# Kernel tuning notes

Hardware: AMD Instinct MI355X
Metric: run time of the kernel (lower is better)

## Reference

```python
import jax, jax.numpy as jnp
import numpy as np

B, V, LP, LO = 256, 128000, 1024, 256


def setup_inputs() -> dict:
    key = jax.random.key(0)
    ks = jax.random.split(key, 11)
    logits = jax.random.normal(ks[0], (B, V), jnp.float32) * 4.0
    presence_penalties = jax.random.uniform(ks[1], (B,), jnp.float32, 0.0, 0.5)
    frequency_penalties = jax.random.uniform(ks[2], (B,), jnp.float32, 0.0, 0.5)
    repetition_penalties = jax.random.uniform(ks[3], (B,), jnp.float32, 1.0, 1.3)
    temperatures = jax.random.uniform(ks[4], (B,), jnp.float32, 0.5, 1.5)
    top_ps = jax.random.uniform(ks[5], (B,), jnp.float32, 0.8, 1.0)
    top_as = jax.random.uniform(ks[6], (B,), jnp.float32, 0.0, 0.2)
    min_ps = jax.random.uniform(ks[7], (B,), jnp.float32, 0.0, 0.1)
    prompt_tokens = jax.random.randint(ks[8], (B, LP), 0, V, jnp.int32)
    output_tokens = jax.random.randint(ks[9], (B, LO), 0, V, jnp.int32)
    top_ks = jax.random.randint(ks[10], (B,), 1, 2048, jnp.int32)
    return dict(logits=logits, presence_penalties=presence_penalties,
                frequency_penalties=frequency_penalties,
                repetition_penalties=repetition_penalties,
                temperatures=temperatures, top_ps=top_ps, top_as=top_as,
                min_ps=min_ps, prompt_tokens=prompt_tokens,
                output_tokens=output_tokens, top_ks=top_ks)


def _bin_counts(tokens, num_seqs, vocab):
    # scatter-add histogram of token ids per row (torch _get_bin_counts_and_mask)
    rows = jnp.arange(num_seqs)[:, None]
    counts = jnp.zeros((num_seqs, vocab), jnp.int32).at[rows, tokens].add(1)
    return counts, counts > 0


def reference(logits, presence_penalties, frequency_penalties,
              repetition_penalties, temperatures, top_ps, top_as, min_ps,
              prompt_tokens, output_tokens, top_ks):
    num_seqs, vocab = logits.shape

    # ---- _apply_penalties ----
    _, prompt_mask = _bin_counts(prompt_tokens, num_seqs, vocab)
    out_counts, out_mask = _bin_counts(output_tokens, num_seqs, vocab)
    rep = jnp.where(prompt_mask | out_mask, repetition_penalties[:, None], 1.0)
    logits = jnp.where(logits > 0, logits / rep, logits * rep)
    logits = logits - frequency_penalties[:, None] * out_counts.astype(logits.dtype)
    logits = logits - presence_penalties[:, None] * out_mask.astype(logits.dtype)

    # ---- _apply_temperature (static path; dynatemp mins/maxs == 0) ----
    temps = jnp.where(temperatures == 0.0, 1.0, temperatures)
    logits = logits / temps[:, None]

    # ---- _apply_alphabet_soup: top-p / top-k / top-a / min-p ----
    order = jnp.argsort(-logits, axis=-1)               # descending sort order
    logits_sort = jnp.take_along_axis(logits, order, axis=-1)
    probs_sort = jax.nn.softmax(logits_sort, axis=-1)
    probs_sum = jnp.cumsum(probs_sort, axis=-1) - probs_sort  # exclusive cumsum
    p_top = probs_sort[:, :1]
    threshold = jnp.maximum(p_top * min_ps[:, None],
                            (p_top * p_top) * top_as[:, None])
    mask = (probs_sort < threshold) | (probs_sum > top_ps[:, None])
    mask = mask.at[:, 0].set(False)                     # always keep argmax
    mask = mask | (jnp.arange(vocab)[None, :] >= top_ks[:, None])  # per-row top-k
    logits_sort = jnp.where(mask, -jnp.inf, logits_sort)

    inv = jnp.argsort(order, axis=-1)                   # inverse permutation
    return jnp.take_along_axis(logits_sort, inv, axis=-1)
```

## Files before the change

### kernel.cpp

```cpp
#include <hip/hip_runtime.h>
#include <hip/hip_fp16.h>
#include <cstdint>

#define NV 128000
#define NROWS 256
#define NLP 1024
#define NLO 256
#define HASH_SZ 4096
#define HEMPTY 0xFFFFFFFFu
#define NBINS 2048
#define GCAP 4096
#define M0 40.0f
#define LOG2E 1.44269504f
#define MASK16 0xFBFFu
#define MASK32 0xFBFFFBFFu

#define HIST_BYTES (NROWS * NBINS * 4)
#define WS_ZERO_BYTES (HIST_BYTES + NROWS * 4)

__device__ __forceinline__ int lbin(float l) {
    int b = (int)((l + 32.0f) * 32.0f);
    return max(0, min(b, NBINS - 1));
}

__device__ __forceinline__ float dec_bf16(uint32_t b) {
    union { uint32_t u; float f; } c; c.u = b << 16; return c.f;
}
__device__ __forceinline__ float dec_fp16(uint32_t h) {
    uint32_t s = h >> 15, e = (h >> 10) & 31u, m = h & 1023u;
    union { uint32_t u; float f; } c;
    if (e == 0) { c.u = (s << 31) | (103u << 23); return c.f * (float)m; }
    if (e == 31) return s ? -65504.0f : 65504.0f;
    c.u = (s << 31) | ((e + 112u) << 23) | (m << 13);
    return c.f;
}
__device__ __forceinline__ float ldf(const void* p, size_t i, int mode) {
    if (mode == 0) return ((const float*)p)[i];
    uint32_t h = ((const unsigned short*)p)[i];
    return (mode == 1) ? dec_bf16(h) : dec_fp16(h);
}
__device__ __forceinline__ uint32_t enc_fp16_safe(float r) {
    if (!(r == r)) r = 0.0f;
    if (r >  65504.0f) r =  65504.0f;
    if (r < -65504.0f) r = -65504.0f;
    uint32_t b = __half_as_ushort(__float2half(r));
    if ((b & 0x7C00u) == 0x7C00u) b = (b & 0x8000u) ? MASK16 : 0x7BFFu;
    return b;
}
__device__ __forceinline__ int sniff_mode(const void* logits) {
    const unsigned short* w = (const unsigned short*)logits;
    int bf = 0, fp = 0;
    for (int i = 0; i < 128; ++i) {
        uint32_t h = w[i];
        uint32_t e8 = (h >> 7) & 0xFFu;
        uint32_t e5 = (h >> 10) & 0x1Fu;
        if (e8 >= 110 && e8 <= 142) bf++;
        if (e5 >= 8 && e5 <= 22) fp++;
    }
    return (bf >= 109) ? 1 : ((fp >= 109) ? 2 : 0);
}

__device__ __forceinline__ void hash_insert(uint32_t* keys, uint32_t* vals,
                                            uint32_t token, uint32_t addv, uint32_t orv) {
    uint32_t h = (token * 2654435761u) & (HASH_SZ - 1);
    while (true) {
        uint32_t k = keys[h];
        if (k == token) break;
        if (k == HEMPTY) {
            uint32_t old = atomicCAS(&keys[h], HEMPTY, token);
            if (old == HEMPTY || old == token) break;
        }
        h = (h + 1) & (HASH_SZ - 1);
    }
    if (addv) atomicAdd(&vals[h], addv);
    if (orv)  atomicOr(&vals[h], orv);
}
__device__ __forceinline__ bool hash_contains(const uint32_t* keys, uint32_t token) {
    uint32_t h = (token * 2654435761u) & (HASH_SZ - 1);
    while (true) {
        uint32_t k = keys[h];
        if (k == token) return true;
        if (k == HEMPTY) return false;
        h = (h + 1) & (HASH_SZ - 1);
    }
}

__device__ __forceinline__ float blk_sum(float v, float* red, int tid) {
    #pragma unroll
    for (int o = 32; o > 0; o >>= 1) v += __shfl_down(v, o, 64);
    __syncthreads();
    if ((tid & 63) == 0) red[tid >> 6] = v;
    __syncthreads();
    if (tid < 64) {
        float w = (tid < 16) ? red[tid] : 0.0f;
        #pragma unroll
        for (int o = 8; o > 0; o >>= 1) w += __shfl_down(w, o, 64);
        if (tid == 0) red[0] = w;
    }
    __syncthreads();
    return red[0];
}
__device__ __forceinline__ int blk_imin(int v, int* red, int tid) {
    #pragma unroll
    for (int o = 32; o > 0; o >>= 1) v = min(v, __shfl_down(v, o, 64));
    __syncthreads();
    if ((tid & 63) == 0) red[tid >> 6] = v;
    __syncthreads();
    if (tid < 64) {
        int w = (tid < 16) ? red[tid] : 0x7FFFFFFF;
        #pragma unroll
        for (int o = 8; o > 0; o >>= 1) w = min(w, __shfl_down(w, o, 64));
        if (tid == 0) red[0] = w;
    }
    __syncthreads();
    return red[0];
}

__global__ __launch_bounds__(256) void k1_hist_z(
    const void* __restrict__ logits,
    const void* __restrict__ temperature,
    uint32_t* __restrict__ hist,
    float* __restrict__ zrow)
{
    const int row  = blockIdx.x >> 2;
    const int part = blockIdx.x & 3;
    const int tid  = threadIdx.x;

    __shared__ uint32_t h4[4][NBINS];
    __shared__ float sred[4];
    __shared__ int s_mode;
    if (tid == 0) s_mode = sniff_mode(logits);
    uint32_t* hw = h4[tid >> 6];
    for (int i = tid; i < 4 * NBINS; i += 256) ((uint32_t*)h4)[i] = 0u;
    __syncthreads();
    const int mode = s_mode;

    float temp = ldf(temperature, row, mode);
    if (temp == 0.0f) temp = 1.0f;
    const float c1 = (1.0f / temp) * LOG2E;
    const float c0 = -M0 * LOG2E;

    float zs = 0.0f;
    const int base = part * 32000;
    if (mode == 0) {
        const float4* l4 = (const float4*)((const float*)logits + (size_t)row * NV + base);
        for (int i = tid; i < 8000; i += 256) {
            float4 f = l4[i];
            zs += exp2f(fmaf(f.x, c1, c0)); atomicAdd(&hw[lbin(f.x)], 1u);
            zs += exp2f(fmaf(f.y, c1, c0)); atomicAdd(&hw[lbin(f.y)], 1u);
            zs += exp2f(fmaf(f.z, c1, c0)); atomicAdd(&hw[lbin(f.z)], 1u);
            zs += exp2f(fmaf(f.w, c1, c0)); atomicAdd(&hw[lbin(f.w)], 1u);
        }
    } else {
        for (int i = tid; i < 32000; i += 256) {
            float l = ldf(logits, (size_t)row * NV + base + i, mode);
            zs += exp2f(fmaf(l, c1, c0)); atomicAdd(&hw[lbin(l)], 1u);
        }
    }
    #pragma unroll
    for (int o = 32; o > 0; o >>= 1) zs += __shfl_down(zs, o, 64);
    __syncthreads();
    if ((tid & 63) == 0) sred[tid >> 6] = zs;
    __syncthreads();
    if (tid == 0) atomicAdd(&zrow[row], sred[0] + sred[1] + sred[2] + sred[3]);

    uint32_t* gh = hist + (size_t)row * NBINS;
    for (int j = tid; j < NBINS; j += 256) {
        uint32_t s = h4[0][j] + h4[1][j] + h4[2][j] + h4[3][j];
        if (s) atomicAdd(&gh[j], s);
    }
}

__global__ __launch_bounds__(1024) void k2_select(
    const void* __restrict__ logits,
    const void* __restrict__ presence,
    const void* __restrict__ frequency,
    const void* __restrict__ repetition,
    const void* __restrict__ temperature,
    const void* __restrict__ top_ps,
    const void* __restrict__ top_as,
    const void* __restrict__ min_ps,
    const int*  __restrict__ prompt_tokens,
    const int*  __restrict__ output_tokens,
    const int*  __restrict__ top_ks,
    const uint32_t* __restrict__ hist,
    const float* __restrict__ zrow,
    unsigned short* __restrict__ out)
{
    const int row = blockIdx.x;
    const int tid = threadIdx.x;

    __shared__ uint32_t hkey[HASH_SZ];
    __shared__ uint32_t hval[HASH_SZ];
    __shared__ float    g_x[GCAP];
    __shared__ int      g_i[GCAP];
    __shared__ uint32_t sS[NBINS];
    __shared__ float red[16];
    __shared__ int s_mode, s_bstar, s_gcnt, s_nkeep, s_sortn;

    if (tid == 0) { s_mode = sniff_mode(logits); s_gcnt = 0; s_bstar = NBINS - 1; }
    for (int i = tid; i < HASH_SZ; i += 1024) { hkey[i] = HEMPTY; hval[i] = 0u; }
    {
        const uint32_t* gh = hist + (size_t)row * NBINS;
        for (int j = tid; j < NBINS; j += 1024) sS[j] = gh[NBINS - 1 - j];
    }
    __syncthreads();
    const int mode = s_mode;

    {
        const int* ot = output_tokens + row * NLO;
        for (int i = tid; i < NLO; i += 1024)
            hash_insert(hkey, hval, (uint32_t)ot[i], 1u, 0u);
        const int* pt = prompt_tokens + row * NLP;
        for (int i = tid; i < NLP; i += 1024)
            hash_insert(hkey, hval, (uint32_t)pt[i], 0u, 0x10000u);
    }
    __syncthreads();

    const float rep  = ldf(repetition, row, mode);
    const float freq = ldf(frequency, row, mode);
    const float pres = ldf(presence, row, mode);
    float temp = ldf(temperature, row, mode);
    if (temp == 0.0f) temp = 1.0f;
    const float tinv = 1.0f / temp;

    float zd = 0.0f;
    for (int s = tid; s < HASH_SZ; s += 1024) {
        uint32_t k = hkey[s];
        if (k != HEMPTY) {
            float l = ldf(logits, (size_t)row * NV + k, mode);
            uint32_t v = hval[s];
            float pl = (l > 0.0f) ? (l / rep) : (l * rep);
            uint32_t cnt = v & 0xFFFFu;
            if (cnt) pl = pl - freq * (float)cnt - pres;
            int bo = lbin(l), bn = lbin(pl);
            if (bo != bn) {
                atomicSub(&sS[NBINS - 1 - bo], 1u);
                atomicAdd(&sS[NBINS - 1 - bn], 1u);
            }
            zd += __expf(pl * tinv - M0) - __expf(l * tinv - M0);
            hval[s] = __float_as_uint(pl);
        }
    }
    const float Z = zrow[row] + blk_sum(zd, red, tid);
    const float invZ = 1.0f / Z;

    int K = top_ks[row];
    if (K < 1) K = 1;
    if (K > 2047) K = 2047;

    for (int d = 1; d < NBINS; d <<= 1) {
        int j0 = tid, j1 = tid + 1024;
        uint32_t a0 = (j0 >= d) ? sS[j0 - d] : 0u;
        uint32_t a1 = (j1 >= d) ? sS[j1 - d] : 0u;
        __syncthreads();
        sS[j0] += a0; sS[j1] += a1;
        __syncthreads();
    }
    {
        int j0 = tid, j1 = tid + 1024;
        uint32_t c0 = sS[j0], p0 = (j0 > 0) ? sS[j0 - 1] : 0u;
        uint32_t c1 = sS[j1], p1 = sS[j1 - 1];
        if (c0 >= (uint32_t)K && (j0 == 0 || p0 < (uint32_t)K)) s_bstar = NBINS - 1 - j0;
        if (c1 >= (uint32_t)K && p1 < (uint32_t)K)             s_bstar = NBINS - 1 - j1;
    }
    __syncthreads();
    const int bstar = s_bstar;

    if (mode == 0) {
        const float4* l4 = (const float4*)((const float*)logits + (size_t)row * NV);
        for (int i = tid; i < NV / 4; i += 1024) {
            float4 f = l4[i];
            int base = i * 4;
            #define GA(val, idx)                                               \
                if (lbin(val) >= bstar && !hash_contains(hkey, (uint32_t)(idx))) { \
                    int pos = atomicAdd(&s_gcnt, 1);                           \
                    if (pos < GCAP) { g_x[pos] = (val) * tinv; g_i[pos] = (idx); } }
            GA(f.x, base + 0) GA(f.y, base + 1) GA(f.z, base + 2) GA(f.w, base + 3)
            #undef GA
        }
    } else {
        for (int i = tid; i < NV; i += 1024) {
            float l = ldf(logits, (size_t)row * NV + i, mode);
            if (lbin(l) >= bstar && !hash_contains(hkey, (uint32_t)i)) {
                int pos = atomicAdd(&s_gcnt, 1);
                if (pos < GCAP) { g_x[pos] = l * tinv; g_i[pos] = i; }
            }
        }
    }
    for (int s = tid; s < HASH_SZ; s += 1024) {
        uint32_t k = hkey[s];
        if (k != HEMPTY) {
            float pl = __uint_as_float(hval[s]);
            if (lbin(pl) >= bstar) {
                int pos = atomicAdd(&s_gcnt, 1);
                if (pos < GCAP) { g_x[pos] = pl * tinv; g_i[pos] = (int)k; }
            }
        }
    }
    __syncthreads();
    const int ng = min(s_gcnt, GCAP);
    if (tid == 0) s_sortn = (ng <= 2048) ? 2048 : GCAP;
    __syncthreads();
    const int sortn = s_sortn;
    for (int i = ng + tid; i < sortn; i += 1024) { g_x[i] = -INFINITY; g_i[i] = 0x7FFFFFFF; }

    for (int k = 2; k <= sortn; k <<= 1) {
        for (int j = k >> 1; j > 0; j >>= 1) {
            __syncthreads();
            for (int p = tid; p < sortn / 2; p += 1024) {
                int i0 = 2 * p - (p & (j - 1));
                int i1 = i0 + j;
                bool up = ((i0 & k) == 0);
                float xa = g_x[i0], xb = g_x[i1];
                int ia = g_i[i0], ib = g_i[i1];
                bool aFirst = (xa > xb) || (xa == xb && ia < ib);
                if (aFirst != up) {
                    g_x[i0] = xb; g_x[i1] = xa;
                    g_i[i0] = ib; g_i[i1] = ia;
                }
            }
        }
    }
    __syncthreads();

    float* pp = (float*)sS;
    const float p0 = __expf(g_x[0] - M0) * invZ;
    const float thr = fmaxf(p0 * ldf(min_ps, row, mode),
                            p0 * p0 * ldf(top_as, row, mode));
    const float topp = ldf(top_ps, row, mode);

    float myp0, myp1;
    {
        int r0 = tid, r1 = tid + 1024;
        myp0 = (r0 < sortn) ? __expf(g_x[r0] - M0) * invZ : 0.0f;
        myp1 = (r1 < sortn) ? __expf(g_x[r1] - M0) * invZ : 0.0f;
        pp[r0] = myp0; pp[r1] = myp1;
    }
    __syncthreads();
    for (int d = 1; d < 2048; d <<= 1) {
        int r0 = tid, r1 = tid + 1024;
        float a0 = (r0 >= d) ? pp[r0 - d] : 0.0f;
        float a1 = (r1 >= d) ? pp[r1 - d] : 0.0f;
        __syncthreads();
        pp[r0] += a0; pp[r1] += a1;
        __syncthreads();
    }
    int fm = 0x7FFFFFFF;
    {
        int r0 = tid, r1 = tid + 1024;
        if (r0 >= 1) {
            float cs = pp[r0] - myp0;
            if (myp0 < thr || cs > topp) fm = min(fm, r0);
        }
        {
            float cs = pp[r1] - myp1;
            if (myp1 < thr || cs > topp) fm = min(fm, r1);
        }
    }
    fm = blk_imin(fm, (int*)red, tid);
    if (tid == 0) {
        int nk = min(fm, K);
        if (nk < 1) nk = 1;
        s_nkeep = min(nk, ng);
    }
    __syncthreads();

    unsigned short* orow = out + (size_t)row * NV;
    {
        uint4 sv; sv.x = MASK32; sv.y = MASK32; sv.z = MASK32; sv.w = MASK32;
        uint4* o4 = (uint4*)orow;
        for (int i = tid; i < 16000; i += 1024) o4[i] = sv;
    }
    __syncthreads();
    {
        const int nk = s_nkeep;
        for (int r = tid; r < nk; r += 1024)
            orow[g_i[r]] = (unsigned short)enc_fp16_safe(g_x[r]);
    }
}

extern "C" void kernel_launch(void* const* d_in, const int* in_sizes, int n_in,
                              void* d_out, int out_size, void* d_ws, size_t ws_size,
                              hipStream_t stream) {
    uint32_t* hist = (uint32_t*)d_ws;
    float* zrow = (float*)((char*)d_ws + HIST_BYTES);

    hipMemsetAsync(d_ws, 0, WS_ZERO_BYTES, stream);

    k1_hist_z<<<NROWS * 4, 256, 0, stream>>>(d_in[0], d_in[4], hist, zrow);

    k2_select<<<NROWS, 1024, 0, stream>>>(
        d_in[0], d_in[1], d_in[2], d_in[3], d_in[4], d_in[5], d_in[6], d_in[7],
        (const int*)d_in[8], (const int*)d_in[9], (const int*)d_in[10],
        hist, zrow, (unsigned short*)d_out);
}
```

Measured before the change: 359.4 us.

## Move softmax denominator into select pass and use wave-level scans and appends

Computes the softmax normalizer Z in k2's full logits sweep rather than in k1, which drops the zrow buffer and its atomics and leaves k1 as a pure histogram pass. Replaces the shared-memory Hillis-Steele scans over bins and probabilities with wave shuffle scans plus a 16-entry cross-wave scan. Candidate appends now go through one ballot and one atomic per wave instead of one atomic per element. The bitonic sort is sized to the next power of two at or above the candidate count and skips barriers when j < 64. The output mask fill moves ahead of the sweep so its stores overlap the reads. Risk: the sub-64 barrier skip assumes intra-wave lockstep, and it adds exp work to the k2 pass.

```diff
diff --git a/kernel.cpp b/kernel.cpp
--- a/kernel.cpp
+++ b/kernel.cpp
@@ -16,7 +16,6 @@
 #define MASK32 0xFBFFFBFFu
 
 #define HIST_BYTES (NROWS * NBINS * 4)
-#define WS_ZERO_BYTES (HIST_BYTES + NROWS * 4)
 
 __device__ __forceinline__ int lbin(float l) {
     int b = (int)((l + 32.0f) * 32.0f);
@@ -116,18 +115,30 @@
     return red[0];
 }
 
-__global__ __launch_bounds__(256) void k1_hist_z(
+__device__ __forceinline__ void gappend(bool pred, float x, int idx,
+                                        int* gcnt, float* g_x, int* g_i, int lane) {
+    unsigned long long mask = __ballot(pred);
+    if (mask == 0ull) return;
+    int cnt = __popcll(mask);
+    int ldr = __ffsll((unsigned long long)mask) - 1;
+    int base = 0;
+    if (lane == ldr) base = atomicAdd(gcnt, cnt);
+    base = __shfl(base, ldr, 64);
+    if (pred) {
+        int pos = base + __popcll(mask & ((1ull << lane) - 1ull));
+        if (pos < GCAP) { g_x[pos] = x; g_i[pos] = idx; }
+    }
+}
+
+__global__ __launch_bounds__(256) void k1_hist(
     const void* __restrict__ logits,
-    const void* __restrict__ temperature,
-    uint32_t* __restrict__ hist,
-    float* __restrict__ zrow)
+    uint32_t* __restrict__ hist)
 {
     const int row  = blockIdx.x >> 2;
     const int part = blockIdx.x & 3;
     const int tid  = threadIdx.x;
 
     __shared__ uint32_t h4[4][NBINS];
-    __shared__ float sred[4];
     __shared__ int s_mode;
     if (tid == 0) s_mode = sniff_mode(logits);
     uint32_t* hw = h4[tid >> 6];
@@ -135,34 +146,23 @@
     __syncthreads();
     const int mode = s_mode;
 
-    float temp = ldf(temperature, row, mode);
-    if (temp == 0.0f) temp = 1.0f;
-    const float c1 = (1.0f / temp) * LOG2E;
-    const float c0 = -M0 * LOG2E;
-
-    float zs = 0.0f;
     const int base = part * 32000;
     if (mode == 0) {
         const float4* l4 = (const float4*)((const float*)logits + (size_t)row * NV + base);
         for (int i = tid; i < 8000; i += 256) {
             float4 f = l4[i];
-            zs += exp2f(fmaf(f.x, c1, c0)); atomicAdd(&hw[lbin(f.x)], 1u);
-            zs += exp2f(fmaf(f.y, c1, c0)); atomicAdd(&hw[lbin(f.y)], 1u);
-            zs += exp2f(fmaf(f.z, c1, c0)); atomicAdd(&hw[lbin(f.z)], 1u);
-            zs += exp2f(fmaf(f.w, c1, c0)); atomicAdd(&hw[lbin(f.w)], 1u);
+            atomicAdd(&hw[lbin(f.x)], 1u);
+            atomicAdd(&hw[lbin(f.y)], 1u);
+            atomicAdd(&hw[lbin(f.z)], 1u);
+            atomicAdd(&hw[lbin(f.w)], 1u);
         }
     } else {
         for (int i = tid; i < 32000; i += 256) {
             float l = ldf(logits, (size_t)row * NV + base + i, mode);
-            zs += exp2f(fmaf(l, c1, c0)); atomicAdd(&hw[lbin(l)], 1u);
-        }
-    }
-    #pragma unroll
-    for (int o = 32; o > 0; o >>= 1) zs += __shfl_down(zs, o, 64);
-    __syncthreads();
-    if ((tid & 63) == 0) sred[tid >> 6] = zs;
-    __syncthreads();
-    if (tid == 0) atomicAdd(&zrow[row], sred[0] + sred[1] + sred[2] + sred[3]);
+            atomicAdd(&hw[lbin(l)], 1u);
+        }
+    }
+    __syncthreads();
 
     uint32_t* gh = hist + (size_t)row * NBINS;
     for (int j = tid; j < NBINS; j += 256) {
@@ -184,11 +184,12 @@
     const int*  __restrict__ output_tokens,
     const int*  __restrict__ top_ks,
     const uint32_t* __restrict__ hist,
-    const float* __restrict__ zrow,
     unsigned short* __restrict__ out)
 {
-    const int row = blockIdx.x;
-    const int tid = threadIdx.x;
+    const int row  = blockIdx.x;
+    const int tid  = threadIdx.x;
+    const int lane = tid & 63;
+    const int wid  = tid >> 6;
 
     __shared__ uint32_t hkey[HASH_SZ];
     __shared__ uint32_t hval[HASH_SZ];
@@ -196,6 +197,8 @@
     __shared__ int      g_i[GCAP];
     __shared__ uint32_t sS[NBINS];
     __shared__ float red[16];
+    __shared__ uint32_t uws[16], uoff[16];
+    __shared__ float    fws[16], foff[16];
     __shared__ int s_mode, s_bstar, s_gcnt, s_nkeep, s_sortn;
 
     if (tid == 0) { s_mode = sniff_mode(logits); s_gcnt = 0; s_bstar = NBINS - 1; }
@@ -223,8 +226,10 @@
     float temp = ldf(temperature, row, mode);
     if (temp == 0.0f) temp = 1.0f;
     const float tinv = 1.0f / temp;
-
-    float zd = 0.0f;
+    const float c1 = tinv * LOG2E;
+    const float c0 = -M0 * LOG2E;
+
+    float zacc = 0.0f;
     for (int s = tid; s < HASH_SZ; s += 1024) {
         uint32_t k = hkey[s];
         if (k != HEMPTY) {
@@ -238,77 +243,99 @@
                 atomicSub(&sS[NBINS - 1 - bo], 1u);
                 atomicAdd(&sS[NBINS - 1 - bn], 1u);
             }
-            zd += __expf(pl * tinv - M0) - __expf(l * tinv - M0);
+            zacc += __expf(pl * tinv - M0) - __expf(l * tinv - M0);
             hval[s] = __float_as_uint(pl);
         }
     }
-    const float Z = zrow[row] + blk_sum(zd, red, tid);
-    const float invZ = 1.0f / Z;
+    __syncthreads();
 
     int K = top_ks[row];
     if (K < 1) K = 1;
     if (K > 2047) K = 2047;
 
-    for (int d = 1; d < NBINS; d <<= 1) {
-        int j0 = tid, j1 = tid + 1024;
-        uint32_t a0 = (j0 >= d) ? sS[j0 - d] : 0u;
-        uint32_t a1 = (j1 >= d) ? sS[j1 - d] : 0u;
+    {
+        uint32_t v0 = sS[2 * tid], v1 = sS[2 * tid + 1];
+        uint32_t s = v0 + v1;
+        #pragma unroll
+        for (int o = 1; o < 64; o <<= 1) {
+            uint32_t t = __shfl_up(s, o, 64);
+            if (lane >= o) s += t;
+        }
+        if (lane == 63) uws[wid] = s;
         __syncthreads();
-        sS[j0] += a0; sS[j1] += a1;
+        if (tid < 16) {
+            uint32_t w = uws[tid];
+            #pragma unroll
+            for (int o = 1; o < 16; o <<= 1) {
+                uint32_t t = __shfl_up(w, o, 64);
+                if (tid >= o) w += t;
+            }
+            uoff[tid] = w - uws[tid];
+        }
         __syncthreads();
-    }
+        uint32_t incl1 = uoff[wid] + s;
+        uint32_t incl0 = incl1 - v1;
+        uint32_t prev0 = incl0 - v0;
+        uint32_t Ku = (uint32_t)K;
+        if (incl0 >= Ku && (tid == 0 || prev0 < Ku)) s_bstar = NBINS - 1 - 2 * tid;
+        if (incl1 >= Ku && incl0 < Ku)               s_bstar = NBINS - 1 - (2 * tid + 1);
+    }
+    __syncthreads();
+    const int bstar = s_bstar;
+
+    unsigned short* orow = out + (size_t)row * NV;
     {
-        int j0 = tid, j1 = tid + 1024;
-        uint32_t c0 = sS[j0], p0 = (j0 > 0) ? sS[j0 - 1] : 0u;
-        uint32_t c1 = sS[j1], p1 = sS[j1 - 1];
-        if (c0 >= (uint32_t)K && (j0 == 0 || p0 < (uint32_t)K)) s_bstar = NBINS - 1 - j0;
-        if (c1 >= (uint32_t)K && p1 < (uint32_t)K)             s_bstar = NBINS - 1 - j1;
-    }
-    __syncthreads();
-    const int bstar = s_bstar;
-
+        uint4 sv; sv.x = MASK32; sv.y = MASK32; sv.z = MASK32; sv.w = MASK32;
+        uint4* o4 = (uint4*)orow;
+        for (int i = tid; i < 16000; i += 1024) o4[i] = sv;
+    }
+
+    float zs = zacc;
     if (mode == 0) {
         const float4* l4 = (const float4*)((const float*)logits + (size_t)row * NV);
         for (int i = tid; i < NV / 4; i += 1024) {
             float4 f = l4[i];
             int base = i * 4;
-            #define GA(val, idx)                                               \
-                if (lbin(val) >= bstar && !hash_contains(hkey, (uint32_t)(idx))) { \
-                    int pos = atomicAdd(&s_gcnt, 1);                           \
-                    if (pos < GCAP) { g_x[pos] = (val) * tinv; g_i[pos] = (idx); } }
+            #define GA(val, idx) {                                                     \
+                zs += exp2f(fmaf((val), c1, c0));                                      \
+                bool pred = (lbin(val) >= bstar) && !hash_contains(hkey, (uint32_t)(idx)); \
+                gappend(pred, (val) * tinv, (idx), &s_gcnt, g_x, g_i, lane); }
             GA(f.x, base + 0) GA(f.y, base + 1) GA(f.z, base + 2) GA(f.w, base + 3)
             #undef GA
         }
     } else {
         for (int i = tid; i < NV; i += 1024) {
             float l = ldf(logits, (size_t)row * NV + i, mode);
-            if (lbin(l) >= bstar && !hash_contains(hkey, (uint32_t)i)) {
-                int pos = atomicAdd(&s_gcnt, 1);
-                if (pos < GCAP) { g_x[pos] = l * tinv; g_i[pos] = i; }
-            }
+            zs += exp2f(fmaf(l, c1, c0));
+            bool pred = (lbin(l) >= bstar) && !hash_contains(hkey, (uint32_t)i);
+            gappend(pred, l * tinv, i, &s_gcnt, g_x, g_i, lane);
         }
     }
     for (int s = tid; s < HASH_SZ; s += 1024) {
         uint32_t k = hkey[s];
-        if (k != HEMPTY) {
-            float pl = __uint_as_float(hval[s]);
-            if (lbin(pl) >= bstar) {
-                int pos = atomicAdd(&s_gcnt, 1);
-                if (pos < GCAP) { g_x[pos] = pl * tinv; g_i[pos] = (int)k; }
-            }
-        }
-    }
-    __syncthreads();
+        bool pred = (k != HEMPTY);
+        float pl = 0.0f;
+        if (pred) {
+            pl = __uint_as_float(hval[s]);
+            pred = (lbin(pl) >= bstar);
+        }
+        gappend(pred, pl * tinv, (int)k, &s_gcnt, g_x, g_i, lane);
+    }
+    __syncthreads();
+
     const int ng = min(s_gcnt, GCAP);
-    if (tid == 0) s_sortn = (ng <= 2048) ? 2048 : GCAP;
-    __syncthreads();
+    if (tid == 0) { int sn = 64; while (sn < ng) sn <<= 1; s_sortn = sn; }
+    const float Z = blk_sum(zs, red, tid);
+    const float invZ = 1.0f / Z;
     const int sortn = s_sortn;
-    for (int i = ng + tid; i < sortn; i += 1024) { g_x[i] = -INFINITY; g_i[i] = 0x7FFFFFFF; }
+    const int padend = (sortn > 2048) ? GCAP : 2048;
+    for (int i = ng + tid; i < padend; i += 1024) { g_x[i] = -INFINITY; g_i[i] = 0x7FFFFFFF; }
+    __syncthreads();
 
     for (int k = 2; k <= sortn; k <<= 1) {
         for (int j = k >> 1; j > 0; j >>= 1) {
-            __syncthreads();
-            for (int p = tid; p < sortn / 2; p += 1024) {
+            if (j >= 64) __syncthreads();
+            for (int p = tid; p < (sortn >> 1); p += 1024) {
                 int i0 = 2 * p - (p & (j - 1));
                 int i1 = i0 + j;
                 bool up = ((i0 & k) == 0);
@@ -324,41 +351,38 @@
     }
     __syncthreads();
 
-    float* pp = (float*)sS;
     const float p0 = __expf(g_x[0] - M0) * invZ;
     const float thr = fmaxf(p0 * ldf(min_ps, row, mode),
                             p0 * p0 * ldf(top_as, row, mode));
     const float topp = ldf(top_ps, row, mode);
 
-    float myp0, myp1;
-    {
-        int r0 = tid, r1 = tid + 1024;
-        myp0 = (r0 < sortn) ? __expf(g_x[r0] - M0) * invZ : 0.0f;
-        myp1 = (r1 < sortn) ? __expf(g_x[r1] - M0) * invZ : 0.0f;
-        pp[r0] = myp0; pp[r1] = myp1;
-    }
-    __syncthreads();
-    for (int d = 1; d < 2048; d <<= 1) {
-        int r0 = tid, r1 = tid + 1024;
-        float a0 = (r0 >= d) ? pp[r0 - d] : 0.0f;
-        float a1 = (r1 >= d) ? pp[r1 - d] : 0.0f;
-        __syncthreads();
-        pp[r0] += a0; pp[r1] += a1;
-        __syncthreads();
-    }
-    int fm = 0x7FFFFFFF;
-    {
-        int r0 = tid, r1 = tid + 1024;
-        if (r0 >= 1) {
-            float cs = pp[r0] - myp0;
-            if (myp0 < thr || cs > topp) fm = min(fm, r0);
-        }
-        {
-            float cs = pp[r1] - myp1;
-            if (myp1 < thr || cs > topp) fm = min(fm, r1);
-        }
-    }
-    fm = blk_imin(fm, (int*)red, tid);
+    float q0 = __expf(g_x[2 * tid]     - M0) * invZ;
+    float q1 = __expf(g_x[2 * tid + 1] - M0) * invZ;
+    float fs = q0 + q1;
+    #pragma unroll
+    for (int o = 1; o < 64; o <<= 1) {
+        float t = __shfl_up(fs, o, 64);
+        if (lane >= o) fs += t;
+    }
+    if (lane == 63) fws[wid] = fs;
+    __syncthreads();
+    if (tid < 16) {
+        float w = fws[tid];
+        #pragma unroll
+        for (int o = 1; o < 16; o <<= 1) {
+            float t = __shfl_up(w, o, 64);
+            if (tid >= o) w += t;
+        }
+        foff[tid] = w - fws[tid];
+    }
+    __syncthreads();
+    float incl1 = foff[wid] + fs;
+    float cs1   = incl1 - q1;
+    float cs0   = cs1 - q0;
+    int fmv = 0x7FFFFFFF;
+    if (tid > 0 && (q0 < thr || cs0 > topp)) fmv = 2 * tid;
+    else if (q1 < thr || cs1 > topp)         fmv = 2 * tid + 1;
+    const int fm = blk_imin(fmv, (int*)red, tid);
     if (tid == 0) {
         int nk = min(fm, K);
         if (nk < 1) nk = 1;
@@ -366,13 +390,6 @@
     }
     __syncthreads();
 
-    unsigned short* orow = out + (size_t)row * NV;
-    {
-        uint4 sv; sv.x = MASK32; sv.y = MASK32; sv.z = MASK32; sv.w = MASK32;
-        uint4* o4 = (uint4*)orow;
-        for (int i = tid; i < 16000; i += 1024) o4[i] = sv;
-    }
-    __syncthreads();
     {
         const int nk = s_nkeep;
         for (int r = tid; r < nk; r += 1024)
@@ -384,14 +401,13 @@
                               void* d_out, int out_size, void* d_ws, size_t ws_size,
                               hipStream_t stream) {
     uint32_t* hist = (uint32_t*)d_ws;
-    float* zrow = (float*)((char*)d_ws + HIST_BYTES);
-
-    hipMemsetAsync(d_ws, 0, WS_ZERO_BYTES, stream);
-
-    k1_hist_z<<<NROWS * 4, 256, 0, stream>>>(d_in[0], d_in[4], hist, zrow);
+
+    hipMemsetAsync(d_ws, 0, HIST_BYTES, stream);
+
+    k1_hist<<<NROWS * 4, 256, 0, stream>>>(d_in[0], hist);
 
     k2_select<<<NROWS, 1024, 0, stream>>>(
         d_in[0], d_in[1], d_in[2], d_in[3], d_in[4], d_in[5], d_in[6], d_in[7],
         (const int*)d_in[8], (const int*)d_in[9], (const int*)d_in[10],
-        hist, zrow, (unsigned short*)d_out);
-}
+        hist, (unsigned short*)d_out);
+}
```

Result: no change. 366.5 us (+2.0%).
